# Optimization experiments

Hardware: AMD Instinct MI355X
Metric: run time of the kernel (lower is better)

The kernel has to match this reference:

```python
import jax, jax.numpy as jnp
import numpy as np

MIN_NORM = 1e-15
BALL_EPS = 1e-5  # projection margin for the Poincare ball


def _tanh(x):
    return jnp.tanh(jnp.clip(x, -15.0, 15.0))


def _artanh(x):
    return jnp.arctanh(jnp.clip(x, -1.0 + 1e-5, 1.0 - 1e-5))


def givens_rotations(r, x):
    # r, x: (N, d) with d even -> (N, d)
    g = r.reshape(r.shape[0], -1, 2)
    g = g / jnp.maximum(jnp.linalg.norm(g, axis=-1, keepdims=True), MIN_NORM)
    xp = x.reshape(x.shape[0], -1, 2)
    swap = jnp.concatenate([-xp[..., 1:], xp[..., :1]], axis=-1)
    return (g[..., :1] * xp + g[..., 1:] * swap).reshape(r.shape[0], -1)


def givens_reflection(r, x):
    g = r.reshape(r.shape[0], -1, 2)
    g = g / jnp.maximum(jnp.linalg.norm(g, axis=-1, keepdims=True), MIN_NORM)
    xp = x.reshape(x.shape[0], -1, 2)
    a = jnp.concatenate([xp[..., :1], -xp[..., 1:]], axis=-1)
    b = jnp.concatenate([xp[..., 1:], xp[..., :1]], axis=-1)
    return (g[..., :1] * a + g[..., 1:] * b).reshape(r.shape[0], -1)


def expmap0(u, c):
    sqrt_c = jnp.sqrt(c)
    u_norm = jnp.maximum(jnp.linalg.norm(u, axis=-1, keepdims=True), MIN_NORM)
    return _tanh(sqrt_c * u_norm) * u / (sqrt_c * u_norm)


def mobius_add(x, y, c):
    x2 = jnp.sum(x * x, -1, keepdims=True)
    y2 = jnp.sum(y * y, -1, keepdims=True)
    xy = jnp.sum(x * y, -1, keepdims=True)
    num = (1 + 2 * c * xy + c * y2) * x + (1 - c * x2) * y
    denom = 1 + 2 * c * xy + c * c * x2 * y2
    return num / jnp.maximum(denom, MIN_NORM)


def project(x, c):
    norm = jnp.maximum(jnp.linalg.norm(x, axis=-1, keepdims=True), MIN_NORM)
    maxnorm = (1.0 - BALL_EPS) / jnp.sqrt(c)
    return jnp.where(norm > maxnorm, x / norm * maxnorm, x)


def hyp_distance_multi_c_bmm(x, v, c):
    # x: (nc, cs, d) queries; v: (nc, ns, d) candidates; c: (nc, cs, 1) curvatures
    sqrt_c = jnp.sqrt(c)                                              # (nc, cs, 1)
    vnorm = jnp.linalg.norm(v, axis=-1, keepdims=True).transpose(0, 2, 1)  # (nc, 1, ns)
    xv = jnp.einsum('bcd,bnd->bcn', x, v) / vnorm                     # (nc, cs, ns)
    gamma = _tanh(sqrt_c * vnorm) / sqrt_c                            # (nc, cs, ns)
    x2 = jnp.sum(x * x, -1, keepdims=True)                            # (nc, cs, 1)
    c1 = 1 - 2 * c * gamma * xv + c * gamma ** 2
    c2 = 1 - c * x2
    num = jnp.sqrt(jnp.maximum(c1 ** 2 * x2 + c2 ** 2 * gamma ** 2 - 2 * c1 * c2 * gamma * xv, 0.0))
    denom = 1 - 2 * c * gamma * xv + c ** 2 * gamma ** 2 * x2
    dist = _artanh(sqrt_c * num / jnp.maximum(denom, MIN_NORM))
    return 2 * dist / sqrt_c                                          # (nc, cs, ns)


def setup_inputs() -> dict:
    key = jax.random.key(0)
    nc, cs, ns, d = 16, 1024, 1024, 512
    B = nc * cs
    ks = jax.random.split(key, 8)
    return {
        'head': jax.random.normal(ks[0], (B, d), jnp.float32),
        'head_bias': jax.random.normal(ks[1], (B, 1), jnp.float32),
        'rel': jax.random.normal(ks[2], (B, d), jnp.float32),
        'rel_diag': jax.random.normal(ks[3], (B, 2 * d), jnp.float32),
        'curvature': jax.random.normal(ks[4], (B, 1), jnp.float32),
        'context': jax.random.normal(ks[5], (B, d), jnp.float32),
        'scale': jnp.full((1,), 1.0 / np.sqrt(d), jnp.float32),
        'tail': jax.random.normal(ks[6], (nc * ns, d), jnp.float32),
        'tail_bias': jax.random.normal(ks[7], (nc * ns, 1), jnp.float32),
        'chunk_size': cs,
        'neg_sample_size': ns,
    }


def reference(head, head_bias, rel, rel_diag, curvature, context, scale, tail,
              tail_bias, chunk_size, neg_sample_size):
    num_chunk = head.shape[0] // chunk_size
    d = head.shape[-1]
    c = jax.nn.softplus(curvature)                                    # (B, 1)
    rot_mat, ref_mat = jnp.split(rel_diag, 2, axis=-1)
    rot_q = givens_rotations(rot_mat, head)[:, None, :]               # (B, 1, d)
    ref_q = givens_reflection(ref_mat, head)[:, None, :]              # (B, 1, d)
    cands = jnp.concatenate([ref_q, rot_q], axis=1)                   # (B, 2, d)
    att_w = jax.nn.softmax(
        jnp.sum(context[:, None, :] * cands * scale, -1, keepdims=True), axis=1)
    att_q = jnp.sum(att_w * cands, axis=1)                            # (B, d)
    lhs = expmap0(att_q, c)
    rel_h = expmap0(rel, c)
    res = project(mobius_add(lhs, rel_h, c), c)                       # (B, d)
    x = res.reshape(num_chunk, chunk_size, d)
    v = tail.reshape(num_chunk, neg_sample_size, d)
    c3 = c.reshape(num_chunk, chunk_size, 1)
    dist = hyp_distance_multi_c_bmm(x, v, c3)                         # (nc, cs, ns)
    score = (-dist ** 2
             + head_bias.reshape(num_chunk, chunk_size, 1)
             + tail_bias.reshape(num_chunk, 1, neg_sample_size))
    return score
```

## Files before the change

kernel.cpp:

```cpp
#include <hip/hip_runtime.h>
#include <math.h>

#define DEV static __device__ __forceinline__

constexpr float MIN_NORM = 1e-15f;
constexpr float BALL_EPS = 1e-5f;
constexpr int D = 512;

typedef float f32x4 __attribute__((ext_vector_type(4)));
typedef short short8v __attribute__((ext_vector_type(8)));
typedef unsigned short ushort8v __attribute__((ext_vector_type(8)));

DEV float wave_sum(float v) {
#pragma unroll
    for (int o = 32; o > 0; o >>= 1) v += __shfl_xor(v, o, 64);
    return v;
}

DEV float rcpf_(float x) { return __builtin_amdgcn_rcpf(x); }
DEV float rsqf_(float x) { return __builtin_amdgcn_rsqf(x); }

DEV float tanh_over_a_pos(float a) {
    const float e = __expf(-2.0f * a);
    return (1.0f - e) * rcpf_((1.0f + e) * fmaxf(a, 1e-20f));
}

DEV unsigned short f2bf(float f) {
    unsigned int u = __float_as_uint(f);
    u = (u + 0x7FFFu + ((u >> 16) & 1u)) >> 16;
    return (unsigned short)u;
}
DEV float bf2f(unsigned short h) { return __uint_as_float(((unsigned int)h) << 16); }

DEV void write_packed_row(unsigned short* pack, size_t nrow, int row,
                          int lane, ushort8v hi, ushort8v lo)
{
    const int kb  = lane >> 2;
    const int cch = lane & 3;
    const int rx  = row & 7;
    unsigned short* dst = pack + ((size_t)kb * nrow + row) * 64;
    *(ushort8v*)(dst + ((cch ^ rx) * 8))       = hi;
    *(ushort8v*)(dst + (((cch + 4) ^ rx) * 8)) = lo;
}

__global__ __launch_bounds__(256)
void prep_kernel(const float* __restrict__ head,
                 const float* __restrict__ rel,
                 const float* __restrict__ rel_diag,
                 const float* __restrict__ curvature,
                 const float* __restrict__ context,
                 const float* __restrict__ scale_p,
                 const float* __restrict__ tail,
                 unsigned short* __restrict__ packA,
                 unsigned short* __restrict__ packB,
                 float* __restrict__ row_x2,
                 float* __restrict__ row_c,
                 float* __restrict__ row_sc,
                 float* __restrict__ vnorm,
                 int B, int T)
{
    const int lane = threadIdx.x & 63;
    const int base = lane * 8;
    const int grow = blockIdx.x * 4 + (threadIdx.x >> 6);

    if (grow >= B) {
        const int row = grow - B;
        const size_t roff = (size_t)row * D + base;
        float v[8];
        *(float4*)&v[0] = *(const float4*)(tail + roff);
        *(float4*)&v[4] = *(const float4*)(tail + roff + 4);
        float s = 0.0f;
        ushort8v hi, lo;
#pragma unroll
        for (int e = 0; e < 8; ++e) {
            s += v[e]*v[e];
            const unsigned short hb_ = f2bf(v[e]);
            hi[e] = hb_;
            lo[e] = f2bf(v[e] - bf2f(hb_));
        }
        s = wave_sum(s);
        write_packed_row(packB, (size_t)T, row, lane, hi, lo);
        if (lane == 0) vnorm[row] = sqrtf(s);
        return;
    }

    const int row = grow;
    const size_t roff = (size_t)row * D;
    const size_t doff = (size_t)row * 2 * D;

    float hv[8], rv[8], gv[8], fv[8], cxv[8];
    *(float4*)&hv[0]  = *(const float4*)(head + roff + base);
    *(float4*)&hv[4]  = *(const float4*)(head + roff + base + 4);
    *(float4*)&rv[0]  = *(const float4*)(rel + roff + base);
    *(float4*)&rv[4]  = *(const float4*)(rel + roff + base + 4);
    *(float4*)&gv[0]  = *(const float4*)(rel_diag + doff + base);
    *(float4*)&gv[4]  = *(const float4*)(rel_diag + doff + base + 4);
    *(float4*)&fv[0]  = *(const float4*)(rel_diag + doff + D + base);
    *(float4*)&fv[4]  = *(const float4*)(rel_diag + doff + D + base + 4);
    *(float4*)&cxv[0] = *(const float4*)(context + roff + base);
    *(float4*)&cxv[4] = *(const float4*)(context + roff + base + 4);

    float rq[8], rf[8];
#pragma unroll
    for (int p = 0; p < 4; ++p) {
        const float x0 = hv[2*p], x1 = hv[2*p+1];
        float g0 = gv[2*p], g1 = gv[2*p+1];
        const float gi = rsqf_(fmaxf(g0*g0 + g1*g1, 1e-30f));
        g0 *= gi; g1 *= gi;
        rq[2*p]   = g0*x0 - g1*x1;
        rq[2*p+1] = g0*x1 + g1*x0;
        float f0 = fv[2*p], f1 = fv[2*p+1];
        const float fi = rsqf_(fmaxf(f0*f0 + f1*f1, 1e-30f));
        f0 *= fi; f1 *= fi;
        rf[2*p]   = f0*x0 + f1*x1;
        rf[2*p+1] = f1*x0 - f0*x1;
    }

    float s0=0,s1=0,s2=0,s3=0,s4=0,s5=0,s6=0,s7=0;
#pragma unroll
    for (int e = 0; e < 8; ++e) {
        s0 += cxv[e]*rf[e];   s1 += cxv[e]*rq[e];
        s2 += rv[e]*rv[e];    s3 += rf[e]*rv[e];
        s4 += rq[e]*rv[e];    s5 += rf[e]*rf[e];
        s6 += rq[e]*rq[e];    s7 += rf[e]*rq[e];
    }
    s0 = wave_sum(s0); s1 = wave_sum(s1); s2 = wave_sum(s2); s3 = wave_sum(s3);
    s4 = wave_sum(s4); s5 = wave_sum(s5); s6 = wave_sum(s6); s7 = wave_sum(s7);

    const float cu = curvature[row];
    const float c  = fmaxf(cu, 0.0f) + __logf(1.0f + __expf(-fabsf(cu)));
    const float sqc = sqrtf(c);
    const float sc  = scale_p[0];

    const float a0 = s0 * sc, a1 = s1 * sc;
    const float mx = fmaxf(a0, a1);
    const float e0 = __expf(a0 - mx), e1 = __expf(a1 - mx);
    const float w0 = e0 * rcpf_(e0 + e1);
    const float w1 = 1.0f - w0;

    const float att2    = fmaxf(w0*w0*s5 + 2.0f*w0*w1*s7 + w1*w1*s6, 0.0f);
    const float attdrel = w0*s3 + w1*s4;
    const float u_att = fmaxf(sqrtf(att2), MIN_NORM);
    const float u_rel = fmaxf(sqrtf(s2), MIN_NORM);

    const float kl = tanh_over_a_pos(sqc * u_att);
    const float kr = tanh_over_a_pos(sqc * u_rel);

    const float x2 = kl*kl*att2;
    const float y2 = kr*kr*s2;
    const float xy = kl*kr*attdrel;

    const float Am  = 1.0f + 2.0f*c*xy + c*y2;
    const float Bm  = 1.0f - c*x2;
    const float inv_den = rcpf_(fmaxf(1.0f + 2.0f*c*xy + c*c*x2*y2, MIN_NORM));

    float pre[8];
    float r2p = 0.0f;
#pragma unroll
    for (int e = 0; e < 8; ++e) {
        const float attq = w0*rf[e] + w1*rq[e];
        pre[e] = (Am*kl*attq + Bm*kr*rv[e]) * inv_den;
        r2p += pre[e]*pre[e];
    }
    r2p = wave_sum(r2p);

    const float nrm  = fmaxf(sqrtf(r2p), MIN_NORM);
    const float maxn = (1.0f - BALL_EPS) * rcpf_(sqc);
    const float psc  = (nrm > maxn) ? (maxn * rcpf_(nrm)) : 1.0f;

    ushort8v hi, lo;
#pragma unroll
    for (int e = 0; e < 8; ++e) {
        const float o = pre[e] * psc;
        const unsigned short hb_ = f2bf(o);
        hi[e] = hb_;
        lo[e] = f2bf(o - bf2f(hb_));
    }
    write_packed_row(packA, (size_t)B, row, lane, hi, lo);

    if (lane == 0) {
        row_x2[row] = r2p * psc * psc;
        row_c[row]  = c;
        row_sc[row] = sqc;
    }
}

__global__ __launch_bounds__(512, 2)
void score_kernel(const unsigned short* __restrict__ packA,
                  const unsigned short* __restrict__ packB,
                  const float* __restrict__ vnorm,
                  const float* __restrict__ row_x2,
                  const float* __restrict__ row_c,
                  const float* __restrict__ row_sc,
                  const float* __restrict__ head_bias,
                  const float* __restrict__ tail_bias,
                  float* __restrict__ out,
                  int cs, int ns, int nrowA, int nrowB)
{
    extern __shared__ __align__(16) char smem[];

    const int orig = blockIdx.x;
    const int wg = (orig & 7) * 32 + (orig >> 3);
    const int bz = wg >> 4;
    const int by = (wg >> 2) & 3;
    const int bx = wg & 3;
    const int m0 = by * 256;
    const int n0 = bx * 256;

    const int tid  = threadIdx.x;
    const int lane = tid & 63;
    const int w    = tid >> 6;
    const int wr   = w >> 2, wn = w & 3;
    const int lrow = lane & 15, lg = lane >> 4;

    f32x4 acc[8][4];
#pragma unroll
    for (int i = 0; i < 8; ++i)
#pragma unroll
        for (int j = 0; j < 4; ++j) acc[i][j] = f32x4{0.f, 0.f, 0.f, 0.f};

    const int xr = (lg ^ (lrow & 7)) * 16;
    const int baseA = (wr * 128 + lrow) * 128 + xr;
    const int baseB = 32768 + (wn * 64 + lrow) * 128 + xr;

    const int s16 = (tid & 255) * 16;
    const int shi = tid >> 8;

    const char* gA = (const char*)packA + (size_t)(bz * cs + m0) * 128;
    const char* gB = (const char*)packB + (size_t)(bz * ns + n0) * 128;
    const size_t strA = (size_t)nrowA * 128;
    const size_t strB = (size_t)nrowB * 128;

#define GLL(srcp, dstp)                                                        \
    __builtin_amdgcn_global_load_lds(                                          \
        (const __attribute__((address_space(1))) unsigned int*)(srcp),         \
        (__attribute__((address_space(3))) unsigned int*)(dstp), 16, 0, 0)

#define STAGE(dstbase, srcpanel, off0, sstr)                                   \
    do { const int o_ = (off0) + s16 + shi * (sstr);                           \
         GLL((srcpanel) + o_, (dstbase) + o_); } while (0)

#define STAGE_A0(d, s) do { STAGE(d, s, 0, 4096);     STAGE(d, s, 16384, 4096); } while (0)
#define STAGE_A1(d, s) do { STAGE(d, s, 8192, 4096);  STAGE(d, s, 24576, 4096); } while (0)
#define STAGE_B0(d, s) do { STAGE(d, s, 0, 8192);     STAGE(d, s, 16384, 8192); } while (0)
#define STAGE_B1(d, s) do { STAGE(d, s, 4096, 8192);  STAGE(d, s, 20480, 8192); } while (0)

#define RD(p, off) (*(const short8v*)((p) + (off)))
#define MFMA_(A_, B_, C_) __builtin_amdgcn_mfma_f32_16x16x32_bf16(A_, B_, C_, 0, 0, 0)

#define QUAD(MOFF, NOFF)                                                       \
    do {                                                                       \
        _Pragma("unroll") for (int mm = 0; mm < 4; ++mm)                       \
        _Pragma("unroll") for (int nn = 0; nn < 2; ++nn)                       \
            acc[(MOFF)+mm][(NOFF)+nn] = MFMA_(ah[mm], bh[(NOFF)+nn], acc[(MOFF)+mm][(NOFF)+nn]); \
        _Pragma("unroll") for (int mm = 0; mm < 4; ++mm)                       \
        _Pragma("unroll") for (int nn = 0; nn < 2; ++nn)                       \
            acc[(MOFF)+mm][(NOFF)+nn] = MFMA_(ah[mm], bl[(NOFF)+nn], acc[(MOFF)+mm][(NOFF)+nn]); \
        _Pragma("unroll") for (int mm = 0; mm < 4; ++mm)                       \
        _Pragma("unroll") for (int nn = 0; nn < 2; ++nn)                       \
            acc[(MOFF)+mm][(NOFF)+nn] = MFMA_(al[mm], bh[(NOFF)+nn], acc[(MOFF)+mm][(NOFF)+nn]); \
    } while (0)

#define BAR()   __builtin_amdgcn_s_barrier()
#define PRIO(x) __builtin_amdgcn_s_setprio(x)

    STAGE_A0(smem, gA);               STAGE_A1(smem, gA);
    STAGE_B0(smem + 32768, gB);       STAGE_B1(smem + 32768, gB);
    STAGE_A0(smem + 65536, gA + strA);
    STAGE_B0(smem + 98304, gB + strB);
    STAGE_B1(smem + 98304, gB + strB);
    asm volatile("s_waitcnt vmcnt(6)" ::: "memory");
    BAR();

    short8v ah[4], al[4], bh[4], bl[4];

#pragma unroll 1
    for (int t = 0; t < 16; ++t) {
        char* cur = smem + (t & 1) * 65536;
        char* oth = smem + ((t + 1) & 1) * 65536;
        const char* gA1 = gA + (size_t)(t + 1) * strA;
        const char* gA2 = gA + (size_t)(t + 2) * strA;
        const char* gB2 = gB + (size_t)(t + 2) * strB;

        if (t < 15) STAGE_A1(oth, gA1);
#pragma unroll
        for (int m = 0; m < 4; ++m) {
            ah[m] = RD(cur, baseA + m * 2048);
            al[m] = RD(cur, (baseA ^ 64) + m * 2048);
        }
#pragma unroll
        for (int n = 0; n < 2; ++n) {
            bh[n] = RD(cur, baseB + n * 2048);
            bl[n] = RD(cur, (baseB ^ 64) + n * 2048);
        }
        BAR(); PRIO(1); QUAD(0, 0); PRIO(0); BAR();

        if (t < 14) STAGE_A0(cur, gA2);
#pragma unroll
        for (int n = 2; n < 4; ++n) {
            bh[n] = RD(cur, baseB + n * 2048);
            bl[n] = RD(cur, (baseB ^ 64) + n * 2048);
        }
        BAR(); PRIO(1); QUAD(0, 2); PRIO(0); BAR();

        if (t < 14) STAGE_B0(cur + 32768, gB2);
#pragma unroll
        for (int m = 0; m < 4; ++m) {
            ah[m] = RD(cur, baseA + 8192 + m * 2048);
            al[m] = RD(cur, (baseA ^ 64) + 8192 + m * 2048);
        }
        BAR(); PRIO(1); QUAD(4, 2); PRIO(0); BAR();

        if (t < 14) STAGE_B1(cur + 32768, gB2);
        BAR(); PRIO(1); QUAD(4, 0); PRIO(0);

        if (t <= 13)      asm volatile("s_waitcnt vmcnt(6)" ::: "memory");
        else if (t == 14) asm volatile("s_waitcnt vmcnt(0)" ::: "memory");
        BAR();
    }

    const int nbase = n0 + wn * 64 + lrow;
    float rvn[4], vnv[4], tb[4];
#pragma unroll
    for (int j = 0; j < 4; ++j) {
        const int gn = bz * ns + nbase + j * 16;
        const float vn = vnorm[gn];
        vnv[j] = vn;
        rvn[j] = 1.0f / vn;
        tb[j]  = tail_bias[gn];
    }
#pragma unroll
    for (int i = 0; i < 8; ++i) {
#pragma unroll
        for (int q = 0; q < 4; ++q) {
            const int gm = bz * cs + m0 + wr * 128 + i * 16 + lg * 4 + q;
            const float x2  = row_x2[gm];
            const float cc  = row_c[gm];
            const float scq = row_sc[gm];
            const float hb  = head_bias[gm];
            const float rscq = 1.0f / scq;
            float* orow = out + (size_t)gm * ns + nbase;
#pragma unroll
            for (int j = 0; j < 4; ++j) {
                const float xv = acc[i][j][q] * rvn[j];
                float xx = fminf(scq * vnv[j], 15.0f);
                const float ey = __expf(2.0f * xx);
                const float g  = (1.0f - 2.0f / (ey + 1.0f)) * rscq;
                const float c1 = 1.0f - 2.0f*cc*g*xv + cc*g*g;
                const float c2 = 1.0f - cc*x2;
                const float num = sqrtf(fmaxf(c1*c1*x2 + c2*c2*g*g - 2.0f*c1*c2*g*xv, 0.0f));
                const float den = fmaxf(1.0f - 2.0f*cc*g*xv + cc*cc*g*g*x2, MIN_NORM);
                float tt = scq * num * __builtin_amdgcn_rcpf(den);
                tt = fminf(tt, 1.0f - 1e-5f);
                const float ath = 0.5f * __logf((1.0f + tt) * __builtin_amdgcn_rcpf(1.0f - tt));
                const float dist = 2.0f * rscq * ath;
                orow[j * 16] = -dist * dist + hb + tb[j];
            }
        }
    }
#undef GLL
#undef STAGE
#undef STAGE_A0
#undef STAGE_A1
#undef STAGE_B0
#undef STAGE_B1
#undef RD
#undef MFMA_
#undef QUAD
#undef BAR
#undef PRIO
}

extern "C" void kernel_launch(void* const* d_in, const int* in_sizes, int n_in,
                              void* d_out, int out_size, void* d_ws, size_t ws_size,
                              hipStream_t stream)
{
    const float* head      = (const float*)d_in[0];
    const float* head_bias = (const float*)d_in[1];
    const float* rel       = (const float*)d_in[2];
    const float* rel_diag  = (const float*)d_in[3];
    const float* curvature = (const float*)d_in[4];
    const float* context   = (const float*)d_in[5];
    const float* scale     = (const float*)d_in[6];
    const float* tail      = (const float*)d_in[7];
    const float* tail_bias = (const float*)d_in[8];

    const int B  = in_sizes[1];
    const int T  = in_sizes[8];
    const int ns = out_size / B;
    const int nc = T / ns;
    const int cs = B / nc;

    unsigned short* packA = (unsigned short*)d_ws;
    unsigned short* packB = packA + (size_t)16 * B * 64;
    float* row_x2 = (float*)(packB + (size_t)16 * T * 64);
    float* row_c  = row_x2 + B;
    float* row_sc = row_c + B;
    float* vnormb = row_sc + B;

    prep_kernel<<<(B + T) / 4, 256, 0, stream>>>(head, rel, rel_diag, curvature,
                                                 context, scale, tail, packA, packB,
                                                 row_x2, row_c, row_sc, vnormb, B, T);

    (void)hipFuncSetAttribute((const void*)score_kernel,
                              hipFuncAttributeMaxDynamicSharedMemorySize, 131072);
    const int nblk = (ns / 256) * (cs / 256) * nc;
    score_kernel<<<nblk, 512, 131072, stream>>>(packA, packB, vnormb, row_x2, row_c,
                                                row_sc, head_bias, tail_bias,
                                                (float*)d_out, cs, ns, B, T);
}
```

Baseline: 130.3 us.

## Pipeline prep rows through LDS and simplify score-kernel double buffering

The prep kernel now gives each block 32 rows and streams them through double-buffered LDS with global_load_lds. The per-row stores are also reorganized into 4-element packed writes. The score kernel drops its fine-grained staggered staging, barriers and setprio in favour of one prefetch of the whole next tile per iteration with a full vmcnt(0) wait. This lowers prep launch overhead and simplifies synchronization, but it may expose more memory latency in the GEMM loop and lowers the prep kernel's parallelism.

```diff
diff --git a/kernel.cpp b/kernel.cpp
--- a/kernel.cpp
+++ b/kernel.cpp
@@ -9,13 +9,7 @@
 
 typedef float f32x4 __attribute__((ext_vector_type(4)));
 typedef short short8v __attribute__((ext_vector_type(8)));
-typedef unsigned short ushort8v __attribute__((ext_vector_type(8)));
-
-DEV float wave_sum(float v) {
-#pragma unroll
-    for (int o = 32; o > 0; o >>= 1) v += __shfl_xor(v, o, 64);
-    return v;
-}
+typedef unsigned short ushort4v __attribute__((ext_vector_type(4)));
 
 DEV float rcpf_(float x) { return __builtin_amdgcn_rcpf(x); }
 DEV float rsqf_(float x) { return __builtin_amdgcn_rsqf(x); }
@@ -32,16 +26,29 @@
 }
 DEV float bf2f(unsigned short h) { return __uint_as_float(((unsigned int)h) << 16); }
 
-DEV void write_packed_row(unsigned short* pack, size_t nrow, int row,
-                          int lane, ushort8v hi, ushort8v lo)
+DEV void write_pack4(unsigned short* pack, size_t nrow, int row, int kbase,
+                     const float* p4)
 {
-    const int kb  = lane >> 2;
-    const int cch = lane & 3;
-    const int rx  = row & 7;
+    const int kb   = kbase >> 5;
+    const int cch  = (kbase >> 3) & 3;
+    const int half = (kbase >> 2) & 1;
+    const int rx   = row & 7;
     unsigned short* dst = pack + ((size_t)kb * nrow + row) * 64;
-    *(ushort8v*)(dst + ((cch ^ rx) * 8))       = hi;
-    *(ushort8v*)(dst + (((cch + 4) ^ rx) * 8)) = lo;
-}
+    ushort4v hi, lo;
+#pragma unroll
+    for (int e = 0; e < 4; ++e) {
+        const unsigned short h_ = f2bf(p4[e]);
+        hi[e] = h_;
+        lo[e] = f2bf(p4[e] - bf2f(h_));
+    }
+    *(ushort4v*)(dst + ((cch     ^ rx) * 8) + half * 4) = hi;
+    *(ushort4v*)(dst + (((cch+4) ^ rx) * 8) + half * 4) = lo;
+}
+
+#define GLLP(srcp, dstp)                                                       \
+    __builtin_amdgcn_global_load_lds(                                          \
+        (const __attribute__((address_space(1))) unsigned int*)(srcp),         \
+        (__attribute__((address_space(3))) unsigned int*)(dstp), 16, 0, 0)
 
 __global__ __launch_bounds__(256)
 void prep_kernel(const float* __restrict__ head,
@@ -59,130 +66,186 @@
                  float* __restrict__ vnorm,
                  int B, int T)
 {
-    const int lane = threadIdx.x & 63;
-    const int base = lane * 8;
-    const int grow = blockIdx.x * 4 + (threadIdx.x >> 6);
-
-    if (grow >= B) {
-        const int row = grow - B;
-        const size_t roff = (size_t)row * D + base;
-        float v[8];
-        *(float4*)&v[0] = *(const float4*)(tail + roff);
-        *(float4*)&v[4] = *(const float4*)(tail + roff + 4);
-        float s = 0.0f;
-        ushort8v hi, lo;
+    __shared__ __align__(16) char lds[2][40960];
+    const int tid  = threadIdx.x;
+    const int lane = tid & 63;
+    const int wv   = tid >> 6;
+    const int t16  = tid * 16;
+    const int hbk  = B >> 5;
+    const float sc = scale_p[0];
+
+#define STAGE_HEAD(nb, r4)                                                     \
+    do {                                                                       \
+        const char* sh_ = (const char*)(head + (size_t)(r4) * D);              \
+        const char* sr_ = (const char*)(rel + (size_t)(r4) * D);               \
+        const char* sd_ = (const char*)(rel_diag + (size_t)(r4) * 2 * D);      \
+        const char* sx_ = (const char*)(context + (size_t)(r4) * D);           \
+        GLLP(sh_ + t16,        (nb) + t16);                                    \
+        GLLP(sh_ + 4096 + t16, (nb) + 4096 + t16);                             \
+        GLLP(sr_ + t16,        (nb) + 8192 + t16);                             \
+        GLLP(sr_ + 4096 + t16, (nb) + 8192 + 4096 + t16);                      \
+        GLLP(sd_ + t16,         (nb) + 16384 + t16);                           \
+        GLLP(sd_ + 4096 + t16,  (nb) + 16384 + 4096 + t16);                    \
+        GLLP(sd_ + 8192 + t16,  (nb) + 16384 + 8192 + t16);                    \
+        GLLP(sd_ + 12288 + t16, (nb) + 16384 + 12288 + t16);                   \
+        GLLP(sx_ + t16,        (nb) + 32768 + t16);                            \
+        GLLP(sx_ + 4096 + t16, (nb) + 32768 + 4096 + t16);                     \
+    } while (0)
+
+    if ((int)blockIdx.x >= hbk) {
+        const int t0 = ((int)blockIdx.x - hbk) * 32;
+        {
+            const char* s0 = (const char*)(tail + (size_t)t0 * D);
+            GLLP(s0 + t16, lds[0] + t16);
+            GLLP(s0 + 4096 + t16, lds[0] + 4096 + t16);
+        }
+#pragma unroll 1
+        for (int it = 0; it < 8; ++it) {
+            char* cb = lds[it & 1];
+            __builtin_amdgcn_s_barrier();
+            if (it < 7) {
+                const char* sn = (const char*)(tail + (size_t)(t0 + (it + 1) * 4) * D);
+                char* nb = lds[(it + 1) & 1];
+                GLLP(sn + t16, nb + t16);
+                GLLP(sn + 4096 + t16, nb + 4096 + t16);
+                asm volatile("s_waitcnt vmcnt(2)" ::: "memory");
+            } else {
+                asm volatile("s_waitcnt vmcnt(0)" ::: "memory");
+            }
+            __builtin_amdgcn_s_barrier();
+
+            const int row = t0 + it * 4 + wv;
+            float v[8];
+            *(f32x4*)&v[0] = *(const f32x4*)(cb + wv * 2048 + lane * 16);
+            *(f32x4*)&v[4] = *(const f32x4*)(cb + wv * 2048 + 1024 + lane * 16);
+            float s = 0.f;
+#pragma unroll
+            for (int e = 0; e < 8; ++e) s += v[e] * v[e];
+#pragma unroll
+            for (int o = 32; o > 0; o >>= 1) s += __shfl_xor(s, o, 64);
+            write_pack4(packB, (size_t)T, row, 4 * lane, &v[0]);
+            write_pack4(packB, (size_t)T, row, 256 + 4 * lane, &v[4]);
+            if (lane == 0) vnorm[row] = sqrtf(s);
+        }
+        return;
+    }
+
+    const int r0 = (int)blockIdx.x * 32;
+    STAGE_HEAD(lds[0], r0);
+
+#pragma unroll 1
+    for (int it = 0; it < 8; ++it) {
+        char* cb = lds[it & 1];
+        const int row = r0 + it * 4 + wv;
+        const float cuv = curvature[row];
+        __builtin_amdgcn_s_barrier();
+        if (it < 7) {
+            STAGE_HEAD(lds[(it + 1) & 1], r0 + (it + 1) * 4);
+            asm volatile("s_waitcnt vmcnt(10)" ::: "memory");
+        } else {
+            asm volatile("s_waitcnt vmcnt(0)" ::: "memory");
+        }
+        __builtin_amdgcn_s_barrier();
+
+        const int off0 = wv * 2048 + lane * 16;
+        const int doff = 16384 + wv * 4096 + lane * 16;
+        float hv[8], rv[8], gv[8], fv[8], cxv[8];
+        *(f32x4*)&hv[0]  = *(const f32x4*)(cb + off0);
+        *(f32x4*)&hv[4]  = *(const f32x4*)(cb + off0 + 1024);
+        *(f32x4*)&rv[0]  = *(const f32x4*)(cb + 8192 + off0);
+        *(f32x4*)&rv[4]  = *(const f32x4*)(cb + 8192 + off0 + 1024);
+        *(f32x4*)&gv[0]  = *(const f32x4*)(cb + doff);
+        *(f32x4*)&gv[4]  = *(const f32x4*)(cb + doff + 1024);
+        *(f32x4*)&fv[0]  = *(const f32x4*)(cb + doff + 2048);
+        *(f32x4*)&fv[4]  = *(const f32x4*)(cb + doff + 2048 + 1024);
+        *(f32x4*)&cxv[0] = *(const f32x4*)(cb + 32768 + off0);
+        *(f32x4*)&cxv[4] = *(const f32x4*)(cb + 32768 + off0 + 1024);
+
+        float rq[8], rf[8];
+#pragma unroll
+        for (int p = 0; p < 4; ++p) {
+            const float x0 = hv[2*p], x1 = hv[2*p+1];
+            float g0 = gv[2*p], g1 = gv[2*p+1];
+            const float gi = rsqf_(fmaxf(g0*g0 + g1*g1, 1e-30f));
+            g0 *= gi; g1 *= gi;
+            rq[2*p]   = g0*x0 - g1*x1;
+            rq[2*p+1] = g0*x1 + g1*x0;
+            float f0 = fv[2*p], f1 = fv[2*p+1];
+            const float fi = rsqf_(fmaxf(f0*f0 + f1*f1, 1e-30f));
+            f0 *= fi; f1 *= fi;
+            rf[2*p]   = f0*x0 + f1*x1;
+            rf[2*p+1] = f1*x0 - f0*x1;
+        }
+
+        float s0=0,s1=0,s2=0,s3=0,s4=0,s5=0,s6=0,s7=0;
 #pragma unroll
         for (int e = 0; e < 8; ++e) {
-            s += v[e]*v[e];
-            const unsigned short hb_ = f2bf(v[e]);
-            hi[e] = hb_;
-            lo[e] = f2bf(v[e] - bf2f(hb_));
-        }
-        s = wave_sum(s);
-        write_packed_row(packB, (size_t)T, row, lane, hi, lo);
-        if (lane == 0) vnorm[row] = sqrtf(s);
-        return;
-    }
-
-    const int row = grow;
-    const size_t roff = (size_t)row * D;
-    const size_t doff = (size_t)row * 2 * D;
-
-    float hv[8], rv[8], gv[8], fv[8], cxv[8];
-    *(float4*)&hv[0]  = *(const float4*)(head + roff + base);
-    *(float4*)&hv[4]  = *(const float4*)(head + roff + base + 4);
-    *(float4*)&rv[0]  = *(const float4*)(rel + roff + base);
-    *(float4*)&rv[4]  = *(const float4*)(rel + roff + base + 4);
-    *(float4*)&gv[0]  = *(const float4*)(rel_diag + doff + base);
-    *(float4*)&gv[4]  = *(const float4*)(rel_diag + doff + base + 4);
-    *(float4*)&fv[0]  = *(const float4*)(rel_diag + doff + D + base);
-    *(float4*)&fv[4]  = *(const float4*)(rel_diag + doff + D + base + 4);
-    *(float4*)&cxv[0] = *(const float4*)(context + roff + base);
-    *(float4*)&cxv[4] = *(const float4*)(context + roff + base + 4);
-
-    float rq[8], rf[8];
-#pragma unroll
-    for (int p = 0; p < 4; ++p) {
-        const float x0 = hv[2*p], x1 = hv[2*p+1];
-        float g0 = gv[2*p], g1 = gv[2*p+1];
-        const float gi = rsqf_(fmaxf(g0*g0 + g1*g1, 1e-30f));
-        g0 *= gi; g1 *= gi;
-        rq[2*p]   = g0*x0 - g1*x1;
-        rq[2*p+1] = g0*x1 + g1*x0;
-        float f0 = fv[2*p], f1 = fv[2*p+1];
-        const float fi = rsqf_(fmaxf(f0*f0 + f1*f1, 1e-30f));
-        f0 *= fi; f1 *= fi;
-        rf[2*p]   = f0*x0 + f1*x1;
-        rf[2*p+1] = f1*x0 - f0*x1;
-    }
-
-    float s0=0,s1=0,s2=0,s3=0,s4=0,s5=0,s6=0,s7=0;
-#pragma unroll
-    for (int e = 0; e < 8; ++e) {
-        s0 += cxv[e]*rf[e];   s1 += cxv[e]*rq[e];
-        s2 += rv[e]*rv[e];    s3 += rf[e]*rv[e];
-        s4 += rq[e]*rv[e];    s5 += rf[e]*rf[e];
-        s6 += rq[e]*rq[e];    s7 += rf[e]*rq[e];
-    }
-    s0 = wave_sum(s0); s1 = wave_sum(s1); s2 = wave_sum(s2); s3 = wave_sum(s3);
-    s4 = wave_sum(s4); s5 = wave_sum(s5); s6 = wave_sum(s6); s7 = wave_sum(s7);
-
-    const float cu = curvature[row];
-    const float c  = fmaxf(cu, 0.0f) + __logf(1.0f + __expf(-fabsf(cu)));
-    const float sqc = sqrtf(c);
-    const float sc  = scale_p[0];
-
-    const float a0 = s0 * sc, a1 = s1 * sc;
-    const float mx = fmaxf(a0, a1);
-    const float e0 = __expf(a0 - mx), e1 = __expf(a1 - mx);
-    const float w0 = e0 * rcpf_(e0 + e1);
-    const float w1 = 1.0f - w0;
-
-    const float att2    = fmaxf(w0*w0*s5 + 2.0f*w0*w1*s7 + w1*w1*s6, 0.0f);
-    const float attdrel = w0*s3 + w1*s4;
-    const float u_att = fmaxf(sqrtf(att2), MIN_NORM);
-    const float u_rel = fmaxf(sqrtf(s2), MIN_NORM);
-
-    const float kl = tanh_over_a_pos(sqc * u_att);
-    const float kr = tanh_over_a_pos(sqc * u_rel);
-
-    const float x2 = kl*kl*att2;
-    const float y2 = kr*kr*s2;
-    const float xy = kl*kr*attdrel;
-
-    const float Am  = 1.0f + 2.0f*c*xy + c*y2;
-    const float Bm  = 1.0f - c*x2;
-    const float inv_den = rcpf_(fmaxf(1.0f + 2.0f*c*xy + c*c*x2*y2, MIN_NORM));
-
-    float pre[8];
-    float r2p = 0.0f;
-#pragma unroll
-    for (int e = 0; e < 8; ++e) {
-        const float attq = w0*rf[e] + w1*rq[e];
-        pre[e] = (Am*kl*attq + Bm*kr*rv[e]) * inv_den;
-        r2p += pre[e]*pre[e];
-    }
-    r2p = wave_sum(r2p);
-
-    const float nrm  = fmaxf(sqrtf(r2p), MIN_NORM);
-    const float maxn = (1.0f - BALL_EPS) * rcpf_(sqc);
-    const float psc  = (nrm > maxn) ? (maxn * rcpf_(nrm)) : 1.0f;
-
-    ushort8v hi, lo;
-#pragma unroll
-    for (int e = 0; e < 8; ++e) {
-        const float o = pre[e] * psc;
-        const unsigned short hb_ = f2bf(o);
-        hi[e] = hb_;
-        lo[e] = f2bf(o - bf2f(hb_));
-    }
-    write_packed_row(packA, (size_t)B, row, lane, hi, lo);
-
-    if (lane == 0) {
-        row_x2[row] = r2p * psc * psc;
-        row_c[row]  = c;
-        row_sc[row] = sqc;
-    }
+            s0 += cxv[e]*rf[e];   s1 += cxv[e]*rq[e];
+            s2 += rv[e]*rv[e];    s3 += rf[e]*rv[e];
+            s4 += rq[e]*rv[e];    s5 += rf[e]*rf[e];
+            s6 += rq[e]*rq[e];    s7 += rf[e]*rq[e];
+        }
+#pragma unroll
+        for (int o = 32; o > 0; o >>= 1) {
+            s0 += __shfl_xor(s0, o, 64); s1 += __shfl_xor(s1, o, 64);
+            s2 += __shfl_xor(s2, o, 64); s3 += __shfl_xor(s3, o, 64);
+            s4 += __shfl_xor(s4, o, 64); s5 += __shfl_xor(s5, o, 64);
+            s6 += __shfl_xor(s6, o, 64); s7 += __shfl_xor(s7, o, 64);
+        }
+
+        const float c  = fmaxf(cuv, 0.0f) + __logf(1.0f + __expf(-fabsf(cuv)));
+        const float sqc = sqrtf(c);
+
+        const float a0 = s0 * sc, a1 = s1 * sc;
+        const float mx = fmaxf(a0, a1);
+        const float e0 = __expf(a0 - mx), e1 = __expf(a1 - mx);
+        const float w0 = e0 * rcpf_(e0 + e1);
+        const float w1 = 1.0f - w0;
+
+        const float att2    = fmaxf(w0*w0*s5 + 2.0f*w0*w1*s7 + w1*w1*s6, 0.0f);
+        const float attdrel = w0*s3 + w1*s4;
+        const float u_att = fmaxf(sqrtf(att2), MIN_NORM);
+        const float u_rel = fmaxf(sqrtf(s2), MIN_NORM);
+
+        const float kl = tanh_over_a_pos(sqc * u_att);
+        const float kr = tanh_over_a_pos(sqc * u_rel);
+
+        const float x2 = kl*kl*att2;
+        const float y2 = kr*kr*s2;
+        const float xy = kl*kr*attdrel;
+
+        const float Am  = 1.0f + 2.0f*c*xy + c*y2;
+        const float Bm  = 1.0f - c*x2;
+        const float inv_den = rcpf_(fmaxf(1.0f + 2.0f*c*xy + c*c*x2*y2, MIN_NORM));
+
+        float pre[8];
+        float r2p = 0.f;
+#pragma unroll
+        for (int e = 0; e < 8; ++e) {
+            const float attq = w0*rf[e] + w1*rq[e];
+            pre[e] = (Am*kl*attq + Bm*kr*rv[e]) * inv_den;
+            r2p += pre[e]*pre[e];
+        }
+#pragma unroll
+        for (int o = 32; o > 0; o >>= 1) r2p += __shfl_xor(r2p, o, 64);
+
+        const float nrm  = fmaxf(sqrtf(r2p), MIN_NORM);
+        const float maxn = (1.0f - BALL_EPS) * rcpf_(sqc);
+        const float psc  = (nrm > maxn) ? (maxn * rcpf_(nrm)) : 1.0f;
+
+        float po[8];
+#pragma unroll
+        for (int e = 0; e < 8; ++e) po[e] = pre[e] * psc;
+        write_pack4(packA, (size_t)B, row, 4 * lane, &po[0]);
+        write_pack4(packA, (size_t)B, row, 256 + 4 * lane, &po[4]);
+
+        if (lane == 0) {
+            row_x2[row] = r2p * psc * psc;
+            row_c[row]  = c;
+            row_sc[row] = sqc;
+        }
+    }
+#undef STAGE_HEAD
 }
 
 __global__ __launch_bounds__(512, 2)
@@ -240,10 +303,15 @@
     do { const int o_ = (off0) + s16 + shi * (sstr);                           \
          GLL((srcpanel) + o_, (dstbase) + o_); } while (0)
 
-#define STAGE_A0(d, s) do { STAGE(d, s, 0, 4096);     STAGE(d, s, 16384, 4096); } while (0)
-#define STAGE_A1(d, s) do { STAGE(d, s, 8192, 4096);  STAGE(d, s, 24576, 4096); } while (0)
-#define STAGE_B0(d, s) do { STAGE(d, s, 0, 8192);     STAGE(d, s, 16384, 8192); } while (0)
-#define STAGE_B1(d, s) do { STAGE(d, s, 4096, 8192);  STAGE(d, s, 20480, 8192); } while (0)
+#define STAGE_ALL(dstslot, srcA, srcB)                                         \
+    do {                                                                       \
+        STAGE(dstslot, srcA, 0, 4096);      STAGE(dstslot, srcA, 16384, 4096); \
+        STAGE(dstslot, srcA, 8192, 4096);   STAGE(dstslot, srcA, 24576, 4096); \
+        STAGE((dstslot)+32768, srcB, 0, 8192);                                 \
+        STAGE((dstslot)+32768, srcB, 16384, 8192);                             \
+        STAGE((dstslot)+32768, srcB, 4096, 8192);                              \
+        STAGE((dstslot)+32768, srcB, 20480, 8192);                             \
+    } while (0)
 
 #define RD(p, off) (*(const short8v*)((p) + (off)))
 #define MFMA_(A_, B_, C_) __builtin_amdgcn_mfma_f32_16x16x32_bf16(A_, B_, C_, 0, 0, 0)
@@ -262,14 +330,10 @@
     } while (0)
 
 #define BAR()   __builtin_amdgcn_s_barrier()
-#define PRIO(x) __builtin_amdgcn_s_setprio(x)
-
-    STAGE_A0(smem, gA);               STAGE_A1(smem, gA);
-    STAGE_B0(smem + 32768, gB);       STAGE_B1(smem + 32768, gB);
-    STAGE_A0(smem + 65536, gA + strA);
-    STAGE_B0(smem + 98304, gB + strB);
-    STAGE_B1(smem + 98304, gB + strB);
-    asm volatile("s_waitcnt vmcnt(6)" ::: "memory");
+#define VM0()   asm volatile("s_waitcnt vmcnt(0)" ::: "memory")
+
+    STAGE_ALL(smem, gA, gB);
+    VM0();
     BAR();
 
     short8v ah[4], al[4], bh[4], bl[4];
@@ -278,11 +342,10 @@
     for (int t = 0; t < 16; ++t) {
         char* cur = smem + (t & 1) * 65536;
         char* oth = smem + ((t + 1) & 1) * 65536;
-        const char* gA1 = gA + (size_t)(t + 1) * strA;
-        const char* gA2 = gA + (size_t)(t + 2) * strA;
-        const char* gB2 = gB + (size_t)(t + 2) * strB;
-
-        if (t < 15) STAGE_A1(oth, gA1);
+
+        if (t < 15)
+            STAGE_ALL(oth, gA + (size_t)(t + 1) * strA, gB + (size_t)(t + 1) * strB);
+
 #pragma unroll
         for (int m = 0; m < 4; ++m) {
             ah[m] = RD(cur, baseA + m * 2048);
@@ -293,29 +356,22 @@
             bh[n] = RD(cur, baseB + n * 2048);
             bl[n] = RD(cur, (baseB ^ 64) + n * 2048);
         }
-        BAR(); PRIO(1); QUAD(0, 0); PRIO(0); BAR();
-
-        if (t < 14) STAGE_A0(cur, gA2);
+        QUAD(0, 0);
 #pragma unroll
         for (int n = 2; n < 4; ++n) {
             bh[n] = RD(cur, baseB + n * 2048);
             bl[n] = RD(cur, (baseB ^ 64) + n * 2048);
         }
-        BAR(); PRIO(1); QUAD(0, 2); PRIO(0); BAR();
-
-        if (t < 14) STAGE_B0(cur + 32768, gB2);
+        QUAD(0, 2);
 #pragma unroll
         for (int m = 0; m < 4; ++m) {
             ah[m] = RD(cur, baseA + 8192 + m * 2048);
             al[m] = RD(cur, (baseA ^ 64) + 8192 + m * 2048);
         }
-        BAR(); PRIO(1); QUAD(4, 2); PRIO(0); BAR();
-
-        if (t < 14) STAGE_B1(cur + 32768, gB2);
-        BAR(); PRIO(1); QUAD(4, 0); PRIO(0);
-
-        if (t <= 13)      asm volatile("s_waitcnt vmcnt(6)" ::: "memory");
-        else if (t == 14) asm volatile("s_waitcnt vmcnt(0)" ::: "memory");
+        QUAD(4, 2);
+        QUAD(4, 0);
+
+        VM0();
         BAR();
     }
 
@@ -360,15 +416,12 @@
     }
 #undef GLL
 #undef STAGE
-#undef STAGE_A0
-#undef STAGE_A1
-#undef STAGE_B0
-#undef STAGE_B1
+#undef STAGE_ALL
 #undef RD
 #undef MFMA_
 #undef QUAD
 #undef BAR
-#undef PRIO
+#undef VM0
 }
 
 extern "C" void kernel_launch(void* const* d_in, const int* in_sizes, int n_in,
@@ -398,9 +451,9 @@
     float* row_sc = row_c + B;
     float* vnormb = row_sc + B;
 
-    prep_kernel<<<(B + T) / 4, 256, 0, stream>>>(head, rel, rel_diag, curvature,
-                                                 context, scale, tail, packA, packB,
-                                                 row_x2, row_c, row_sc, vnormb, B, T);
+    prep_kernel<<<(B + T) / 32, 256, 0, stream>>>(head, rel, rel_diag, curvature,
+                                                  context, scale, tail, packA, packB,
+                                                  row_x2, row_c, row_sc, vnormb, B, T);
 
     (void)hipFuncSetAttribute((const void*)score_kernel,
                               hipFuncAttributeMaxDynamicSharedMemorySize, 131072);
```

After: 133.2 us. 2.2% more time.
